# Optimization experiments

Measured on AMD Instinct MI355X. Metric: run time of the kernel, lower is better.

Reference implementation:

```python
import jax, jax.numpy as jnp
import numpy as np

SIMILARITY_EPS = 1e-4
B, N, M, K = 4096, 16384, 12, 2048  # batch, signal length, n ref spectra, spectrum bins


def setup_inputs() -> dict:
    key = jax.random.key(0)
    k1, k2, k3 = jax.random.split(key, 3)
    Y = jax.random.normal(k1, (B, N), dtype=jnp.float32)
    model_spectra = jax.random.uniform(k2, (M, K), dtype=jnp.float32)
    dissonance_vals = jax.random.uniform(k3, (M,), dtype=jnp.float32)
    return {"Y": Y, "model_spectra": model_spectra, "dissonance_vals": dissonance_vals}


def reference(Y, model_spectra, dissonance_vals):
    n = Y.shape[-1]
    k = model_spectra.shape[-1]
    # FFT magnitude spectrum, scaled, truncated to first K bins: [B, K]
    yf = (2.0 / n) * jnp.abs(jnp.fft.fft(Y, axis=-1)[:, :k])
    # Euclidean distance to each reference spectrum via expansion (avoids [B,M,K] intermediate)
    sq = (jnp.sum(yf * yf, axis=-1, keepdims=True)            # [B,1]
          + jnp.sum(model_spectra * model_spectra, axis=-1)   # [M]
          - 2.0 * (yf @ model_spectra.T))                     # [B,M]
    dist = jnp.sqrt(jnp.maximum(sq, 0.0))                     # [B,M]
    sim = 1.0 / (dist + SIMILARITY_EPS)                       # [B,M]
    w = sim / jnp.sum(sim, axis=-1, keepdims=True)            # [B,M]
    out = w @ (1.0 - dissonance_vals)                         # [B]
    return out[:, None]                                       # [B,1]
```

## Files before the change

### kernel.cpp

```cpp
#include <hip/hip_runtime.h>
#include <hip/hip_bf16.h>
#include <math.h>

#define BATCH 4096
#define NSIG  16384
#define MREF  12
#define KBIN  2048

constexpr float SIM_EPS = 1e-4f;
constexpr float TWO_PI = 6.2831853071795864769f;

typedef __attribute__((ext_vector_type(8))) short bfrag;
typedef __attribute__((ext_vector_type(4))) float f32x4;
typedef __attribute__((ext_vector_type(4))) int   i32x4;
typedef __attribute__((ext_vector_type(4))) unsigned u32x4;

__device__ unsigned g_wtab[16 * 256 * 4];
__device__ unsigned g_b2tab[1024 * 4];
__device__ unsigned g_utw[32 * 128 * 4];
__device__ float    g_msn[MREF];

__device__ inline unsigned pkbf(float lo, float hi) {
  unsigned r;
  asm("v_cvt_pk_bf16_f32 %0, %1, %2" : "=v"(r) : "v"(lo), "v"(hi));
  return r;
}
__device__ inline float bflo(unsigned u) { return __builtin_bit_cast(float, u << 16); }
__device__ inline float bfhi(unsigned u) { return __builtin_bit_cast(float, u & 0xffff0000u); }
__device__ inline f32x4 mfma16(bfrag a, bfrag b, f32x4 c) {
  return __builtin_amdgcn_mfma_f32_16x16x32_bf16(a, b, c, 0, 0, 0);
}
__device__ inline int fsw(int n2) { return (n2 ^ (n2 >> 2)) & 7; }

__global__ __launch_bounds__(256) void setup_kernel(const float* __restrict__ ms) {
  const int blk = blockIdx.x, t = threadIdx.x;
  if (blk < 16) {
    const int ri = blk & 1, ks = (blk >> 1) & 3, mt = blk >> 3;
    const int lane = t & 63, w = t >> 6, c = lane & 15, g = lane >> 4;
    const int k1 = 32 * w + 16 * mt + c;
    unsigned wd[4];
    #pragma unroll
    for (int jp = 0; jp < 4; ++jp) {
      float v[2];
      #pragma unroll
      for (int h = 0; h < 2; ++h) {
        const int n1 = 32 * ks + 8 * g + 2 * jp + h;
        const float th = TWO_PI * (float)((k1 * n1) & 127) / 128.f;
        float sn, cs; sincosf(th, &sn, &cs);
        v[h] = ri ? -sn : cs;
      }
      wd[jp] = pkbf(v[0], v[1]);
    }
    *(u32x4*)&g_wtab[(blk * 256 + t) * 4] = (u32x4){wd[0], wd[1], wd[2], wd[3]};
  } else if (blk == 16) {
    #pragma unroll
    for (int r = 0; r < 4; ++r) {
      const int e = t * 4 + r;
      const int lane = e & 63, ri = (e >> 6) & 1, s_ = (e >> 7) & 1, ch = (e >> 8) & 3;
      const int c = lane & 15, g = lane >> 4;
      unsigned wd[4];
      #pragma unroll
      for (int i = 0; i < 4; ++i) {
        const int ang = (c * (32 * ch + 16 * s_ + 4 * g + i)) & 127;
        const float th = TWO_PI * (float)ang / 128.f;
        float sn, cs; sincosf(th, &sn, &cs);
        wd[i] = ri ? pkbf(-sn, cs) : pkbf(cs, sn);
      }
      *(u32x4*)&g_b2tab[e * 4] = (u32x4){wd[0], wd[1], wd[2], wd[3]};
    }
  } else if (blk < 25) {
    const int base = (blk - 17) * 512 + t;
    #pragma unroll
    for (int r = 0; r < 2; ++r) {
      const int e = base + r * 256;
      const int a = e >> 7, n2 = e & 127;
      unsigned wd[4];
      #pragma unroll
      for (int q = 0; q < 4; ++q) {
        const int ang = ((4 * a + q) * n2) & 16383;
        const float th = TWO_PI * (float)ang / 16384.f;
        float sn, cs; sincosf(th, &sn, &cs);
        wd[q] = pkbf(cs, -sn);
      }
      *(u32x4*)&g_utw[e * 4] = (u32x4){wd[0], wd[1], wd[2], wd[3]};
    }
  } else {
    const int m = blk - 25;
    if (m < MREF) {
      float p = 0.f;
      for (int i = t; i < KBIN; i += 256) { float v = ms[m * KBIN + i]; p += v * v; }
      #pragma unroll
      for (int o = 32; o; o >>= 1) p += __shfl_xor(p, o, 64);
      __shared__ float r4[4];
      if ((t & 63) == 0) r4[t >> 6] = p;
      __syncthreads();
      if (t == 0) g_msn[m] = r4[0] + r4[1] + r4[2] + r4[3];
    }
  }
}

__global__ __launch_bounds__(256, 4) void consonance_kernel(
    const float* __restrict__ Y, const float* __restrict__ ms,
    const float* __restrict__ diss, float* __restrict__ out) {
  __shared__ __align__(16) unsigned short Ysb[128 * 128];
  __shared__ __align__(16) unsigned Ua[4 * 32 * 32];
  __shared__ float red[4][13];

  const int t = threadIdx.x;
  const int b = blockIdx.x;
  const int lane = t & 63;
  const int w = t >> 6;
  const int g = lane >> 4;
  const int c = lane & 15;

  bfrag Wr[2][4], Wi[2][4];
  #pragma unroll
  for (int mt = 0; mt < 2; ++mt)
    #pragma unroll
    for (int ks = 0; ks < 4; ++ks) {
      Wr[mt][ks] = *(const bfrag*)&g_wtab[(((mt * 4 + ks) * 2 + 0) * 256 + t) * 4];
      Wi[mt][ks] = *(const bfrag*)&g_wtab[(((mt * 4 + ks) * 2 + 1) * 256 + t) * 4];
    }
  u32x4 utwP[2][2];
  #pragma unroll
  for (int nt = 0; nt < 2; ++nt)
    #pragma unroll
    for (int mt = 0; mt < 2; ++mt) {
      const int a = 8 * w + 4 * mt + g;
      utwP[nt][mt] = *(const u32x4*)&g_utw[(a * 128 + (16 * nt + c)) * 4];
    }

  {
    const int c0 = (t & 31) << 2;
    const int h  = t >> 5;
    const float* yrow = Y + (size_t)b * NSIG + c0;
    #pragma unroll
    for (int u = 0; u < 2; ++u) {
      float4 v[8];
      #pragma unroll
      for (int r = 0; r < 8; ++r)
        v[r] = *(const float4*)(yrow + 128 * (16 * h + 8 * u + r));
      #pragma unroll
      for (int cc = 0; cc < 4; ++cc) {
        const int n2 = c0 + cc;
        unsigned p0 = pkbf((&v[0].x)[cc], (&v[1].x)[cc]);
        unsigned p1 = pkbf((&v[2].x)[cc], (&v[3].x)[cc]);
        unsigned p2 = pkbf((&v[4].x)[cc], (&v[5].x)[cc]);
        unsigned p3 = pkbf((&v[6].x)[cc], (&v[7].x)[cc]);
        const int blk = (2 * h + u) ^ fsw(n2);
        *(i32x4*)((char*)Ysb + n2 * 256 + (blk << 4)) =
            (i32x4){(int)p0, (int)p1, (int)p2, (int)p3};
      }
    }
  }

  f32x4 aXr[2] = {{0.f,0.f,0.f,0.f},{0.f,0.f,0.f,0.f}};
  f32x4 aXi[2] = {{0.f,0.f,0.f,0.f},{0.f,0.f,0.f,0.f}};
  unsigned* uw = Ua + (w << 10);

  __syncthreads();

  #pragma unroll
  for (int ch = 0; ch < 4; ++ch) {
    bfrag B2[2][2];
    #pragma unroll
    for (int s = 0; s < 2; ++s) {
      B2[0][s] = *(const bfrag*)&g_b2tab[(((ch * 2 + s) * 2 + 0) * 64 + lane) * 4];
      B2[1][s] = *(const bfrag*)&g_b2tab[(((ch * 2 + s) * 2 + 1) * 64 + lane) * 4];
    }
    u32x4 utwC[2][2];
    #pragma unroll
    for (int nt = 0; nt < 2; ++nt)
      #pragma unroll
      for (int mt = 0; mt < 2; ++mt) utwC[nt][mt] = utwP[nt][mt];
    if (ch < 3) {
      #pragma unroll
      for (int nt = 0; nt < 2; ++nt)
        #pragma unroll
        for (int mt = 0; mt < 2; ++mt) {
          const int a = 8 * w + 4 * mt + g;
          utwP[nt][mt] = *(const u32x4*)&g_utw[(a * 128 + (32 * (ch + 1) + 16 * nt + c)) * 4];
        }
    }
    bfrag bfr[2][4];
    #pragma unroll
    for (int nt = 0; nt < 2; ++nt) {
      const int n2 = 32 * ch + 16 * nt + c;
      #pragma unroll
      for (int ks = 0; ks < 4; ++ks) {
        const int blk = (4 * ks + g) ^ fsw(n2);
        bfr[nt][ks] = *(const bfrag*)((const char*)Ysb + n2 * 256 + (blk << 4));
      }
    }
    f32x4 aTr[2][2] = {{{0.f,0.f,0.f,0.f},{0.f,0.f,0.f,0.f}},
                       {{0.f,0.f,0.f,0.f},{0.f,0.f,0.f,0.f}}};
    f32x4 aTi[2][2] = {{{0.f,0.f,0.f,0.f},{0.f,0.f,0.f,0.f}},
                       {{0.f,0.f,0.f,0.f},{0.f,0.f,0.f,0.f}}};
    #pragma unroll
    for (int mt = 0; mt < 2; ++mt)
      #pragma unroll
      for (int nt = 0; nt < 2; ++nt)
        #pragma unroll
        for (int ks = 0; ks < 4; ++ks) {
          aTr[mt][nt] = mfma16(Wr[mt][ks], bfr[nt][ks], aTr[mt][nt]);
          aTi[mt][nt] = mfma16(Wi[mt][ks], bfr[nt][ks], aTi[mt][nt]);
        }
    #pragma unroll
    for (int nt = 0; nt < 2; ++nt) {
      #pragma unroll
      for (int mt = 0; mt < 2; ++mt) {
        const u32x4 tw = utwC[nt][mt];
        #pragma unroll
        for (int q = 0; q < 4; ++q) {
          const float twr = bflo(tw[q]), twi = bfhi(tw[q]);
          const float tr = aTr[mt][nt][q], ti = aTi[mt][nt][q];
          const float ur = tr * twr - ti * twi;
          const float ui = tr * twi + ti * twr;
          const int rl = 16 * mt + 4 * g + q;
          const int tt = 16 * nt + c;
          uw[rl * 32 + (tt ^ ((rl & 7) << 2))] = pkbf(ur, ui);
        }
      }
    }
    #pragma unroll
    for (int mt = 0; mt < 2; ++mt) {
      const int rl = 16 * mt + c;
      #pragma unroll
      for (int s = 0; s < 2; ++s) {
        const int t4 = (16 * s + 4 * g) ^ ((rl & 7) << 2);
        bfrag af = *(const bfrag*)((const char*)uw + rl * 128 + (t4 << 2));
        aXr[mt] = mfma16(af, B2[0][s], aXr[mt]);
        aXi[mt] = mfma16(af, B2[1][s], aXi[mt]);
      }
    }
  }

  const float scale = 2.0f / (float)NSIG;
  float yfv[2][4], S = 0.f;
  #pragma unroll
  for (int mt = 0; mt < 2; ++mt)
    #pragma unroll
    for (int q = 0; q < 4; ++q) {
      const float xr = aXr[mt][q], xi = aXi[mt][q];
      const float yf = scale * sqrtf(xr * xr + xi * xi);
      yfv[mt][q] = yf;
      S += yf * yf;
    }
  float dot[MREF];
  #pragma unroll
  for (int m = 0; m < MREF; ++m) dot[m] = 0.f;
  const int kb0 = 32 * w + 4 * g + 128 * c;
  #pragma unroll
  for (int m = 0; m < MREF; ++m) {
    #pragma unroll
    for (int mt = 0; mt < 2; ++mt) {
      const float4 mv = *(const float4*)&ms[m * KBIN + kb0 + 16 * mt];
      dot[m] = fmaf(yfv[mt][0], mv.x, dot[m]);
      dot[m] = fmaf(yfv[mt][1], mv.y, dot[m]);
      dot[m] = fmaf(yfv[mt][2], mv.z, dot[m]);
      dot[m] = fmaf(yfv[mt][3], mv.w, dot[m]);
    }
  }
  #pragma unroll
  for (int o = 32; o; o >>= 1) {
    S += __shfl_xor(S, o, 64);
    #pragma unroll
    for (int m = 0; m < MREF; ++m) dot[m] += __shfl_xor(dot[m], o, 64);
  }
  if (lane == 0) {
    red[w][0] = S;
    #pragma unroll
    for (int m = 0; m < MREF; ++m) red[w][1 + m] = dot[m];
  }
  __syncthreads();
  if (t == 0) {
    const float St = red[0][0] + red[1][0] + red[2][0] + red[3][0];
    float ssum = 0.f, wsum = 0.f;
    for (int m = 0; m < MREF; ++m) {
      const float dm = red[0][1 + m] + red[1][1 + m] + red[2][1 + m] + red[3][1 + m];
      const float d2 = St + g_msn[m] - 2.f * dm;
      const float dist = sqrtf(fmaxf(d2, 0.f));
      const float sim = 1.f / (dist + SIM_EPS);
      ssum += sim;
      wsum += sim * (1.f - diss[m]);
    }
    out[b] = wsum / ssum;
  }
}

extern "C" void kernel_launch(void* const* d_in, const int* in_sizes, int n_in,
                              void* d_out, int out_size, void* d_ws, size_t ws_size,
                              hipStream_t stream) {
  const float* Y    = (const float*)d_in[0];
  const float* ms   = (const float*)d_in[1];
  const float* diss = (const float*)d_in[2];
  float* outp = (float*)d_out;
  setup_kernel<<<37, 256, 0, stream>>>(ms);
  consonance_kernel<<<BATCH, 256, 0, stream>>>(Y, ms, diss, outp);
}
```

Baseline: 420.5 us.

## Double-buffer per-chunk Y staging in LDS to overlap global loads with MFMA

Replaces the single up-front load of the whole 128x128 bf16 Y tile into shared memory with a two-slot ring of 32-column chunks. The next chunk's global loads are issued at the start of each iteration, converted and stored into the other slot after the MFMA work, with a barrier per chunk. This halves LDS use, which may help occupancy, and hides global-load latency behind compute. In exchange it adds three block barriers and narrower float2 global loads that coalesce worse.

```diff
diff --git a/kernel.cpp b/kernel.cpp
--- a/kernel.cpp
+++ b/kernel.cpp
@@ -12,7 +12,6 @@
 
 typedef __attribute__((ext_vector_type(8))) short bfrag;
 typedef __attribute__((ext_vector_type(4))) float f32x4;
-typedef __attribute__((ext_vector_type(4))) int   i32x4;
 typedef __attribute__((ext_vector_type(4))) unsigned u32x4;
 
 __device__ unsigned g_wtab[16 * 256 * 4];
@@ -30,7 +29,7 @@
 __device__ inline f32x4 mfma16(bfrag a, bfrag b, f32x4 c) {
   return __builtin_amdgcn_mfma_f32_16x16x32_bf16(a, b, c, 0, 0, 0);
 }
-__device__ inline int fsw(int n2) { return (n2 ^ (n2 >> 2)) & 7; }
+__device__ inline int fj(int j) { return (j & 7) ^ (j >> 3); }
 
 __global__ __launch_bounds__(256) void setup_kernel(const float* __restrict__ ms) {
   const int blk = blockIdx.x, t = threadIdx.x;
@@ -102,7 +101,7 @@
 __global__ __launch_bounds__(256, 4) void consonance_kernel(
     const float* __restrict__ Y, const float* __restrict__ ms,
     const float* __restrict__ diss, float* __restrict__ out) {
-  __shared__ __align__(16) unsigned short Ysb[128 * 128];
+  __shared__ __align__(16) unsigned Yw[2][32 * 64];
   __shared__ __align__(16) unsigned Ua[4 * 32 * 32];
   __shared__ float red[4][13];
 
@@ -112,6 +111,8 @@
   const int w = t >> 6;
   const int g = lane >> 4;
   const int c = lane & 15;
+  const int rr = t >> 4;
+  const int cp = t & 15;
 
   bfrag Wr[2][4], Wi[2][4];
   #pragma unroll
@@ -130,27 +131,20 @@
       utwP[nt][mt] = *(const u32x4*)&g_utw[(a * 128 + (16 * nt + c)) * 4];
     }
 
+  const float* yrow = Y + (size_t)b * NSIG + 2 * cp;
+
   {
-    const int c0 = (t & 31) << 2;
-    const int h  = t >> 5;
-    const float* yrow = Y + (size_t)b * NSIG + c0;
-    #pragma unroll
-    for (int u = 0; u < 2; ++u) {
-      float4 v[8];
-      #pragma unroll
-      for (int r = 0; r < 8; ++r)
-        v[r] = *(const float4*)(yrow + 128 * (16 * h + 8 * u + r));
-      #pragma unroll
-      for (int cc = 0; cc < 4; ++cc) {
-        const int n2 = c0 + cc;
-        unsigned p0 = pkbf((&v[0].x)[cc], (&v[1].x)[cc]);
-        unsigned p1 = pkbf((&v[2].x)[cc], (&v[3].x)[cc]);
-        unsigned p2 = pkbf((&v[4].x)[cc], (&v[5].x)[cc]);
-        unsigned p3 = pkbf((&v[6].x)[cc], (&v[7].x)[cc]);
-        const int blk = (2 * h + u) ^ fsw(n2);
-        *(i32x4*)((char*)Ysb + n2 * 256 + (blk << 4)) =
-            (i32x4){(int)p0, (int)p1, (int)p2, (int)p3};
-      }
+    float2 yv[8];
+    #pragma unroll
+    for (int i = 0; i < 8; ++i) yv[i] = *(const float2*)(yrow + (8 * rr + i) * 128);
+    #pragma unroll
+    for (int cc = 0; cc < 2; ++cc) {
+      const int j = 2 * cp + cc;
+      unsigned w0 = pkbf(cc ? yv[0].y : yv[0].x, cc ? yv[1].y : yv[1].x);
+      unsigned w1 = pkbf(cc ? yv[2].y : yv[2].x, cc ? yv[3].y : yv[3].x);
+      unsigned w2 = pkbf(cc ? yv[4].y : yv[4].x, cc ? yv[5].y : yv[5].x);
+      unsigned w3 = pkbf(cc ? yv[6].y : yv[6].x, cc ? yv[7].y : yv[7].x);
+      *(u32x4*)&Yw[0][j * 64 + ((rr ^ fj(j)) << 2)] = (u32x4){w0, w1, w2, w3};
     }
   }
 
@@ -162,6 +156,13 @@
 
   #pragma unroll
   for (int ch = 0; ch < 4; ++ch) {
+    const int cur = ch & 1;
+    float2 yv[8];
+    if (ch < 3) {
+      #pragma unroll
+      for (int i = 0; i < 8; ++i)
+        yv[i] = *(const float2*)(yrow + (ch + 1) * 32 + (8 * rr + i) * 128);
+    }
     bfrag B2[2][2];
     #pragma unroll
     for (int s = 0; s < 2; ++s) {
@@ -185,12 +186,10 @@
     bfrag bfr[2][4];
     #pragma unroll
     for (int nt = 0; nt < 2; ++nt) {
-      const int n2 = 32 * ch + 16 * nt + c;
-      #pragma unroll
-      for (int ks = 0; ks < 4; ++ks) {
-        const int blk = (4 * ks + g) ^ fsw(n2);
-        bfr[nt][ks] = *(const bfrag*)((const char*)Ysb + n2 * 256 + (blk << 4));
-      }
+      const int j = 16 * nt + c;
+      #pragma unroll
+      for (int ks = 0; ks < 4; ++ks)
+        bfr[nt][ks] = *(const bfrag*)&Yw[cur][j * 64 + (((4 * ks + g) ^ fj(j)) << 2)];
     }
     f32x4 aTr[2][2] = {{{0.f,0.f,0.f,0.f},{0.f,0.f,0.f,0.f}},
                        {{0.f,0.f,0.f,0.f},{0.f,0.f,0.f,0.f}}};
@@ -233,6 +232,18 @@
         aXi[mt] = mfma16(af, B2[1][s], aXi[mt]);
       }
     }
+    if (ch < 3) {
+      #pragma unroll
+      for (int cc = 0; cc < 2; ++cc) {
+        const int j = 2 * cp + cc;
+        unsigned w0 = pkbf(cc ? yv[0].y : yv[0].x, cc ? yv[1].y : yv[1].x);
+        unsigned w1 = pkbf(cc ? yv[2].y : yv[2].x, cc ? yv[3].y : yv[3].x);
+        unsigned w2 = pkbf(cc ? yv[4].y : yv[4].x, cc ? yv[5].y : yv[5].x);
+        unsigned w3 = pkbf(cc ? yv[6].y : yv[6].x, cc ? yv[7].y : yv[7].x);
+        *(u32x4*)&Yw[cur ^ 1][j * 64 + ((rr ^ fj(j)) << 2)] = (u32x4){w0, w1, w2, w3};
+      }
+      __syncthreads();
+    }
   }
 
   const float scale = 2.0f / (float)NSIG;
```

Measured after the change: 628.3 us. 1.49x slower.
